# Kernel optimization log

Hardware: AMD Instinct MI355X
Metric: run time of the kernel (lower is better)

Reference implementation:

```python
import jax, jax.numpy as jnp
import numpy as np

# Config constants (match init_kwargs / config)
B = 16        # config.BATCH_SIZE
T = 2048      # config.TRAIN_LEN
C = 256       # input channels (input_shape[-1])
K = 8         # kernel_size
F = 256       # nb_filters
DIL = 4       # dilation_rate


def setup_inputs() -> dict:
    key = jax.random.key(0)
    k1, k2, k3 = jax.random.split(key, 3)
    inputs = jax.random.normal(k1, (B, T, C), dtype=jnp.float32)
    kernel = jax.random.normal(k2, (C, K, F), dtype=jnp.float32) * 0.05
    bias = jax.random.normal(k3, (F,), dtype=jnp.float32) * 0.05
    return {"inputs": inputs, "kernel": kernel, "bias": bias}


def reference(inputs, kernel, bias):
    # Original TF layer computes, per (b,t,k,f):
    #   raw[b,t,k,f] = sum_c (x[b,t,c] * kernel[c,k,f] + bias[f])
    #               = conv[b,t,k,f] + C * bias[f]
    # (bias is added BEFORE the reduce_sum over the channel axis, so it is
    #  scaled by C — we reproduce that quirk faithfully.)
    # Then each (t,k) slice is scatter-added to output time t + k*dilation
    # (the gather_nd + zero-pad construction in TF implements exactly this
    #  dilated transposed-conv scatter; non-matching positions gather zeros),
    # and finally the last T timesteps are kept.
    Bq, Tq, Cq = inputs.shape
    Kq, Fq = kernel.shape[1], kernel.shape[2]
    conv = jnp.einsum('btc,ckf->btkf', inputs, kernel) + jnp.asarray(Cq, inputs.dtype) * bias
    L = Tq + (Kq - 1) * DIL  # final_time_len
    # scatter positions: out[i + j*DIL] += conv[:, i, j, :]
    pos = (jnp.arange(Tq)[:, None] + DIL * jnp.arange(Kq)[None, :]).reshape(-1)  # (T*K,)
    out = jnp.zeros((Bq, L, Fq), dtype=conv.dtype)
    out = out.at[:, pos, :].add(conv.reshape(Bq, Tq * Kq, Fq))
    return out[:, -Tq:, :]
```

## Files before the change

### kernel.cpp

```cpp
#include <hip/hip_runtime.h>
#include <hip/hip_bf16.h>


#define B_   16
#define T_   2048
#define C_   256
#define KT   8
#define F_   256
#define SH   28
#define BT   128
#define WIN  (BT + SH)
#define AF32_OFF 0
#define ABF_OFF  19968
#define BB_OFF   39936

typedef __attribute__((ext_vector_type(8))) short short8;
typedef __attribute__((ext_vector_type(4))) float floatx4;

__device__ inline void gload16(const void* g, void* l) {
    __builtin_amdgcn_global_load_lds(
        (const __attribute__((address_space(1))) void*)g,
        (__attribute__((address_space(3))) void*)l, 16, 0, 0);
}

__device__ inline short8 cvt8(float4 a, float4 b) {
    float v[8] = {a.x, a.y, a.z, a.w, b.x, b.y, b.z, b.w};
    short8 r;
    #pragma unroll
    for (int i = 0; i < 8; ++i) {
        __hip_bfloat16 h = __float2bfloat16(v[i]);
        r[i] = *reinterpret_cast<const short*>(&h);
    }
    return r;
}

__global__ __launch_bounds__(256) void wprep_kernel(const float* __restrict__ W,
                                                    ushort* __restrict__ Wf) {
    const int o  = blockIdx.x * 256 + threadIdx.x;
    const int gg = o & 511;
    const int tf = o >> 9;
    const int fh = tf & 1;
    const int S  = tf >> 1;
    const int j  = S & 7, c = S >> 3;
    const int fl = gg >> 2, p = gg & 3;
    const int q  = p ^ ((fl >> 1) & 3);
    const int f  = fh * 128 + fl;
    const int c0 = c * 32 + q * 8;
    short8 pk;
    #pragma unroll
    for (int i = 0; i < 8; ++i) {
        __hip_bfloat16 h = __float2bfloat16(W[((c0 + i) * KT + j) * F_ + f]);
        pk[i] = *reinterpret_cast<const short*>(&h);
    }
    *reinterpret_cast<short8*>(Wf + (size_t)o * 8) = pk;
}

__global__ __launch_bounds__(256, 2) void deconv_kernel(
        const float* __restrict__ x, const ushort* __restrict__ Wf,
        const float* __restrict__ bias, float* __restrict__ out) {
    __shared__ alignas(16) char smem[64512];
    const int bid = blockIdx.x;
    const int fh  = bid & 1;
    const int tb  = bid >> 1;
    const int b   = tb & 15;
    const int t0  = (tb >> 4) * BT;
    const int tid = threadIdx.x;
    const int w   = tid >> 6, lane = tid & 63;
    const int l16 = lane & 15, q = lane >> 4;
    const int wm  = w >> 1, wf2 = w & 1;
    const int rA  = wm * 64 + l16;
    const int flb = wf2 * 64 + l16;

    float*  Af = (float*)(smem + AF32_OFF);
    ushort* Ab = (ushort*)(smem + ABF_OFF);
    ushort* Bb = (ushort*)(smem + BB_OFF);

#define VMW(N_) do { asm volatile("s_waitcnt vmcnt(" #N_ ")" ::: "memory"); \
        __builtin_amdgcn_sched_barrier(0); } while (0)
#define LKW() do { asm volatile("s_waitcnt lgkmcnt(0)" ::: "memory");       \
        __builtin_amdgcn_sched_barrier(0); } while (0)
#define BAR() do { __builtin_amdgcn_sched_barrier(0);                       \
        __builtin_amdgcn_s_barrier();                                       \
        asm volatile("" ::: "memory");                                      \
        __builtin_amdgcn_sched_barrier(0); } while (0)

#define A_ROUND(k_, cc_) do {                                               \
        const int u_ = (k_) * 256 + tid;                                    \
        if ((k_) < 4 || u_ < WIN * 8) {                                     \
            const int row_ = u_ >> 3, g_ = u_ & 7;                          \
            int tr_ = t0 + row_; if (tr_ > T_ - 1) tr_ = T_ - 1;            \
            const float* src_ = x + ((size_t)(b * T_ + tr_) * C_ +          \
                                     (cc_) * 32 + g_ * 4);                  \
            gload16(src_, smem + AF32_OFF + ((k_) * 256 + w * 64) * 16);    \
        } } while (0)

#define B_STAGE(S_) do {                                                    \
        const ushort* s0_ = Wf + (((size_t)(S_) * 2 + fh) * 4096);          \
        char* l0_ = smem + BB_OFF + ((S_) % 3) * 8192;                      \
        gload16(s0_ + tid * 8,         l0_ + (w * 64) * 16);                \
        gload16(s0_ + 2048 + tid * 8,  l0_ + (256 + w * 64) * 16);          \
        } while (0)

#define CVT_ROUND(r_, p2_) do {                                             \
        const int task_ = (r_) * 256 + tid;                                 \
        if ((r_) < 2 || task_ < WIN * 4) {                                  \
            const int row_ = task_ >> 2, qq_ = task_ & 3;                   \
            const int pp_ = (qq_ + row_) & 3;                               \
            short8 pk_ = {0, 0, 0, 0, 0, 0, 0, 0};                          \
            if (t0 + row_ < T_) {                                           \
                const float* fp_ = Af + row_ * 32 + pp_ * 8;                \
                float4 u0_ = *(const float4*)fp_;                           \
                float4 u1_ = *(const float4*)(fp_ + 4);                     \
                pk_ = cvt8(u0_, u1_);                                       \
            }                                                               \
            *(short8*)(Ab + (p2_) * 4992 + row_ * 32 +                      \
                       ((pp_ ^ ((row_ >> 1) & 3)) * 8)) = pk_;              \
        } } while (0)

#define MFMA_PHASE(c_, jj_) do {                                            \
        const ushort* ab_ = Ab + ((c_) & 1) * 4992;                         \
        const ushort* bb_ = Bb + ((((c_) * 8 + (jj_)) % 3)) * 4096;         \
        short8 afr_[4], bfr_[4];                                            \
        _Pragma("unroll")                                                   \
        for (int mf = 0; mf < 4; ++mf) {                                    \
            const int row_ = rA + (SH - 4 * (jj_)) + mf * 16;               \
            afr_[mf] = *(const short8*)(ab_ + row_ * 32 +                   \
                        ((q ^ ((row_ >> 1) & 3)) * 8));                     \
        }                                                                   \
        _Pragma("unroll")                                                   \
        for (int nf = 0; nf < 4; ++nf) {                                    \
            const int fl_ = flb + nf * 16;                                  \
            bfr_[nf] = *(const short8*)(bb_ + fl_ * 32 +                    \
                        ((q ^ ((fl_ >> 1) & 3)) * 8));                      \
        }                                                                   \
        __builtin_amdgcn_s_setprio(1);                                      \
        _Pragma("unroll")                                                   \
        for (int mf = 0; mf < 4; ++mf)                                      \
            _Pragma("unroll")                                               \
            for (int nf = 0; nf < 4; ++nf)                                  \
                acc[mf][nf] = __builtin_amdgcn_mfma_f32_16x16x32_bf16(      \
                    afr_[mf], bfr_[nf], acc[mf][nf], 0, 0, 0);              \
        __builtin_amdgcn_s_setprio(0);                                      \
        } while (0)

#define PHASE(jj_, NN_, DOA_, CV_) do {                                     \
        if (DOA_) A_ROUND(jj_, c + 1);                                      \
        B_STAGE(c * 8 + (jj_) + 2);                                         \
        VMW(NN_);                                                           \
        BAR();                                                              \
        MFMA_PHASE(c, jj_);                                                 \
        if ((CV_) == 1) { CVT_ROUND(0, (c + 1) & 1);                        \
                          CVT_ROUND(1, (c + 1) & 1); LKW(); }               \
        if ((CV_) == 2) { CVT_ROUND(2, (c + 1) & 1); LKW(); }               \
        BAR();                                                              \
        } while (0)

#define PHASE7(jj_, NN_, DOB_) do {                                         \
        if (DOB_) B_STAGE(56 + (jj_) + 2);                                  \
        VMW(NN_);                                                           \
        BAR();                                                              \
        MFMA_PHASE(7, jj_);                                                 \
        BAR();                                                              \
        } while (0)

    float bf4[4];
    #pragma unroll
    for (int nf = 0; nf < 4; ++nf) bf4[nf] = bias[fh * 128 + flb + nf * 16];

    floatx4 acc[4][4];
    #pragma unroll
    for (int mf = 0; mf < 4; ++mf)
        #pragma unroll
        for (int nf = 0; nf < 4; ++nf)
            acc[mf][nf] = (floatx4){0.f, 0.f, 0.f, 0.f};

    A_ROUND(0, 0); A_ROUND(1, 0); A_ROUND(2, 0); A_ROUND(3, 0); A_ROUND(4, 0);
    B_STAGE(0); B_STAGE(1);
    VMW(4);
    BAR();
    CVT_ROUND(0, 0); CVT_ROUND(1, 0); CVT_ROUND(2, 0);
    LKW();
    BAR();

    for (int c = 0; c < 7; ++c) {
        PHASE(0, 5, 1, 0);
        PHASE(1, 6, 1, 0);
        PHASE(2, 6, 1, 0);
        PHASE(3, 6, 1, 0);
        PHASE(4, 6, 1, 0);
        PHASE(5, 5, 0, 0);
        PHASE(6, 4, 0, 1);
        PHASE(7, 4, 0, 2);
    }
    PHASE7(0, 4, 1); PHASE7(1, 4, 1); PHASE7(2, 4, 1); PHASE7(3, 4, 1);
    PHASE7(4, 4, 1); PHASE7(5, 4, 1); PHASE7(6, 2, 0); PHASE7(7, 0, 0);

    #pragma unroll
    for (int mf = 0; mf < 4; ++mf) {
        #pragma unroll
        for (int nf = 0; nf < 4; ++nf) {
            const int f = fh * 128 + flb + nf * 16;
            #pragma unroll
            for (int r = 0; r < 4; ++r) {
                const int t = t0 + wm * 64 + mf * 16 + q * 4 + r;
                const int jmin = (t < T_ - SH) ? 0 : (((t - (T_ - SH)) >> 2) + 1);
                out[(size_t)(b * T_ + t) * F_ + f] =
                    acc[mf][nf][r] + (float)(8 - jmin) * 256.0f * bf4[nf];
            }
        }
    }
#undef VMW
#undef LKW
#undef BAR
#undef A_ROUND
#undef B_STAGE
#undef CVT_ROUND
#undef MFMA_PHASE
#undef PHASE
#undef PHASE7
}

extern "C" void kernel_launch(void* const* d_in, const int* in_sizes, int n_in,
                              void* d_out, int out_size, void* d_ws, size_t ws_size,
                              hipStream_t stream) {
    const float* x    = (const float*)d_in[0];
    const float* W    = (const float*)d_in[1];
    const float* bias = (const float*)d_in[2];
    float* out = (float*)d_out;
    ushort* Wf = (ushort*)d_ws;

    wprep_kernel<<<256, 256, 0, stream>>>(W, Wf);
    deconv_kernel<<<512, 256, 0, stream>>>(x, Wf, bias, out);
}
```

Before: 50.58 us.

## Stream weight fragments directly into registers and cut per-tap barriers

Weight fragments are now laid out by wprep in MFMA fragment order and loaded straight into registers with inline global_load_dwordx4, using a 3-slot register ring, instead of being staged through LDS. The fp32 input staging is double-buffered with a rotated layout, so only two barriers per channel chunk remain instead of two per tap. The bf16 conversion is spread across the last taps. This removes LDS traffic and most barrier stalls for B, at the cost of more VGPRs (48 extra for bR) and reliance on hand-counted vmcnt waits.

```diff
diff --git a/kernel.cpp b/kernel.cpp
--- a/kernel.cpp
+++ b/kernel.cpp
@@ -10,12 +10,13 @@
 #define SH   28
 #define BT   128
 #define WIN  (BT + SH)
-#define AF32_OFF 0
-#define ABF_OFF  19968
-#define BB_OFF   39936
+#define FB   19968
+#define ABFB 9984
+#define ABF  (2 * FB)
 
 typedef __attribute__((ext_vector_type(8))) short short8;
 typedef __attribute__((ext_vector_type(4))) float floatx4;
+typedef __attribute__((ext_vector_type(4))) int   intx4;
 
 __device__ inline void gload16(const void* g, void* l) {
     __builtin_amdgcn_global_load_lds(
@@ -36,29 +37,27 @@
 
 __global__ __launch_bounds__(256) void wprep_kernel(const float* __restrict__ W,
                                                     ushort* __restrict__ Wf) {
-    const int o  = blockIdx.x * 256 + threadIdx.x;
-    const int gg = o & 511;
-    const int tf = o >> 9;
-    const int fh = tf & 1;
-    const int S  = tf >> 1;
-    const int j  = S & 7, c = S >> 3;
-    const int fl = gg >> 2, p = gg & 3;
-    const int q  = p ^ ((fl >> 1) & 3);
-    const int f  = fh * 128 + fl;
-    const int c0 = c * 32 + q * 8;
+    const int tid  = threadIdx.x;
+    const int fid  = blockIdx.x * 4 + (tid >> 6);
+    const int lane = tid & 63;
+    const int g    = fid & 15;
+    const int S    = fid >> 4;
+    const int j    = S & 7, c = S >> 3;
+    const int c0   = c * 32 + (lane >> 4) * 8;
+    const int f    = g * 16 + (lane & 15);
     short8 pk;
     #pragma unroll
     for (int i = 0; i < 8; ++i) {
         __hip_bfloat16 h = __float2bfloat16(W[((c0 + i) * KT + j) * F_ + f]);
         pk[i] = *reinterpret_cast<const short*>(&h);
     }
-    *reinterpret_cast<short8*>(Wf + (size_t)o * 8) = pk;
+    *reinterpret_cast<short8*>(Wf + (size_t)fid * 512 + lane * 8) = pk;
 }
 
 __global__ __launch_bounds__(256, 2) void deconv_kernel(
         const float* __restrict__ x, const ushort* __restrict__ Wf,
         const float* __restrict__ bias, float* __restrict__ out) {
-    __shared__ alignas(16) char smem[64512];
+    __shared__ alignas(16) char smem[59904];
     const int bid = blockIdx.x;
     const int fh  = bid & 1;
     const int tb  = bid >> 1;
@@ -68,12 +67,8 @@
     const int w   = tid >> 6, lane = tid & 63;
     const int l16 = lane & 15, q = lane >> 4;
     const int wm  = w >> 1, wf2 = w & 1;
-    const int rA  = wm * 64 + l16;
-    const int flb = wf2 * 64 + l16;
-
-    float*  Af = (float*)(smem + AF32_OFF);
-    ushort* Ab = (ushort*)(smem + ABF_OFF);
-    ushort* Bb = (ushort*)(smem + BB_OFF);
+    const char* wfbase = (const char*)Wf +
+        (size_t)(fh * 8 + wf2 * 4) * 1024 + (size_t)lane * 16;
 
 #define VMW(N_) do { asm volatile("s_waitcnt vmcnt(" #N_ ")" ::: "memory"); \
         __builtin_amdgcn_sched_barrier(0); } while (0)
@@ -86,52 +81,50 @@
 
 #define A_ROUND(k_, cc_) do {                                               \
         const int u_ = (k_) * 256 + tid;                                    \
-        if ((k_) < 4 || u_ < WIN * 8) {                                     \
-            const int row_ = u_ >> 3, g_ = u_ & 7;                          \
+        if ((k_) < 4 || tid < 224) {                                        \
+            const int row_ = u_ >> 3, s_ = u_ & 7;                          \
+            const int v_   = (s_ + 8 - (row_ & 7)) & 7;                     \
             int tr_ = t0 + row_; if (tr_ > T_ - 1) tr_ = T_ - 1;            \
-            const float* src_ = x + ((size_t)(b * T_ + tr_) * C_ +          \
-                                     (cc_) * 32 + g_ * 4);                  \
-            gload16(src_, smem + AF32_OFF + ((k_) * 256 + w * 64) * 16);    \
+            gload16(x + ((size_t)(b * T_ + tr_) * C_ + (cc_) * 32 + v_ * 4),\
+                    smem + ((cc_) & 1) * FB + ((k_) * 256 + w * 64) * 16);  \
         } } while (0)
 
-#define B_STAGE(S_) do {                                                    \
-        const ushort* s0_ = Wf + (((size_t)(S_) * 2 + fh) * 4096);          \
-        char* l0_ = smem + BB_OFF + ((S_) % 3) * 8192;                      \
-        gload16(s0_ + tid * 8,         l0_ + (w * 64) * 16);                \
-        gload16(s0_ + 2048 + tid * 8,  l0_ + (256 + w * 64) * 16);          \
+#define B_ISSUE(S_, sl_) do {                                               \
+        const char* p_ = wfbase + (size_t)(S_) * 16384;                     \
+        asm volatile("global_load_dwordx4 %0, %1, off"                      \
+            : "=v"(bR[sl_][0]) : "v"(p_) : "memory");                       \
+        asm volatile("global_load_dwordx4 %0, %1, off offset:1024"          \
+            : "=v"(bR[sl_][1]) : "v"(p_) : "memory");                       \
+        asm volatile("global_load_dwordx4 %0, %1, off offset:2048"          \
+            : "=v"(bR[sl_][2]) : "v"(p_) : "memory");                       \
+        asm volatile("global_load_dwordx4 %0, %1, off offset:3072"          \
+            : "=v"(bR[sl_][3]) : "v"(p_) : "memory");                       \
         } while (0)
 
-#define CVT_ROUND(r_, p2_) do {                                             \
-        const int task_ = (r_) * 256 + tid;                                 \
-        if ((r_) < 2 || task_ < WIN * 4) {                                  \
-            const int row_ = task_ >> 2, qq_ = task_ & 3;                   \
-            const int pp_ = (qq_ + row_) & 3;                               \
-            short8 pk_ = {0, 0, 0, 0, 0, 0, 0, 0};                          \
-            if (t0 + row_ < T_) {                                           \
-                const float* fp_ = Af + row_ * 32 + pp_ * 8;                \
-                float4 u0_ = *(const float4*)fp_;                           \
-                float4 u1_ = *(const float4*)(fp_ + 4);                     \
-                pk_ = cvt8(u0_, u1_);                                       \
-            }                                                               \
-            *(short8*)(Ab + (p2_) * 4992 + row_ * 32 +                      \
-                       ((pp_ ^ ((row_ >> 1) & 3)) * 8)) = pk_;              \
+#define CVT_ROUND(r_, par_) do {                                            \
+        if ((r_) < 2 || tid < 112) {                                        \
+            const int task_ = (r_) * 256 + tid;                             \
+            const int row_ = task_ >> 2, g_ = task_ & 3;                    \
+            const int s1_ = (2 * g_ + row_) & 7;                            \
+            const int s2_ = (2 * g_ + 1 + row_) & 7;                        \
+            const char* fb_ = smem + (par_) * FB;                           \
+            float4 u0_ = *(const float4*)(fb_ + (row_ * 8 + s1_) * 16);     \
+            float4 u1_ = *(const float4*)(fb_ + (row_ * 8 + s2_) * 16);     \
+            short8 pk_ = {0,0,0,0,0,0,0,0};                                 \
+            if (t0 + row_ < T_) pk_ = cvt8(u0_, u1_);                       \
+            const int p_ = g_ ^ ((row_ >> 1) & 3);                          \
+            *(short8*)(smem + ABF + (par_) * ABFB + (row_ * 4 + p_) * 16)   \
+                = pk_;                                                      \
         } } while (0)
 
-#define MFMA_PHASE(c_, jj_) do {                                            \
-        const ushort* ab_ = Ab + ((c_) & 1) * 4992;                         \
-        const ushort* bb_ = Bb + ((((c_) * 8 + (jj_)) % 3)) * 4096;         \
-        short8 afr_[4], bfr_[4];                                            \
+#define MFMA_TAP(c_, j_) do {                                               \
+        const char* ab_ = smem + ABF + ((c_) & 1) * ABFB;                   \
+        short8 af_[4];                                                      \
         _Pragma("unroll")                                                   \
         for (int mf = 0; mf < 4; ++mf) {                                    \
-            const int row_ = rA + (SH - 4 * (jj_)) + mf * 16;               \
-            afr_[mf] = *(const short8*)(ab_ + row_ * 32 +                   \
-                        ((q ^ ((row_ >> 1) & 3)) * 8));                     \
-        }                                                                   \
-        _Pragma("unroll")                                                   \
-        for (int nf = 0; nf < 4; ++nf) {                                    \
-            const int fl_ = flb + nf * 16;                                  \
-            bfr_[nf] = *(const short8*)(bb_ + fl_ * 32 +                    \
-                        ((q ^ ((fl_ >> 1) & 3)) * 8));                      \
+            const int row_ = wm * 64 + (SH - 4 * (j_)) + mf * 16 + l16;     \
+            const int p_   = q ^ ((row_ >> 1) & 3);                         \
+            af_[mf] = *(const short8*)(ab_ + (row_ * 4 + p_) * 16);         \
         }                                                                   \
         __builtin_amdgcn_s_setprio(1);                                      \
         _Pragma("unroll")                                                   \
@@ -139,33 +132,34 @@
             _Pragma("unroll")                                               \
             for (int nf = 0; nf < 4; ++nf)                                  \
                 acc[mf][nf] = __builtin_amdgcn_mfma_f32_16x16x32_bf16(      \
-                    afr_[mf], bfr_[nf], acc[mf][nf], 0, 0, 0);              \
+                    af_[mf],                                                \
+                    *(short8*)&bR[(((c_) * 8 + (j_)) % 3)][nf],             \
+                    acc[mf][nf], 0, 0, 0);                                  \
         __builtin_amdgcn_s_setprio(0);                                      \
         } while (0)
 
-#define PHASE(jj_, NN_, DOA_, CV_) do {                                     \
-        if (DOA_) A_ROUND(jj_, c + 1);                                      \
-        B_STAGE(c * 8 + (jj_) + 2);                                         \
-        VMW(NN_);                                                           \
+#define CHUNK_STD(c_) do {                                                  \
+        A_ROUND(0, (c_)+1); A_ROUND(1, (c_)+1); A_ROUND(2, (c_)+1);         \
+        A_ROUND(3, (c_)+1); A_ROUND(4, (c_)+1);                             \
+        B_ISSUE((c_)*8+2, (((c_)*8+2)%3)); VMW(13); MFMA_TAP(c_, 0);        \
+        B_ISSUE((c_)*8+3, (((c_)*8+3)%3)); VMW(13); MFMA_TAP(c_, 1);        \
+        B_ISSUE((c_)*8+4, (((c_)*8+4)%3)); VMW(8);  MFMA_TAP(c_, 2);        \
         BAR();                                                              \
-        MFMA_PHASE(c, jj_);                                                 \
-        if ((CV_) == 1) { CVT_ROUND(0, (c + 1) & 1);                        \
-                          CVT_ROUND(1, (c + 1) & 1); LKW(); }               \
-        if ((CV_) == 2) { CVT_ROUND(2, (c + 1) & 1); LKW(); }               \
-        BAR();                                                              \
+        B_ISSUE((c_)*8+5, (((c_)*8+5)%3)); VMW(8);  MFMA_TAP(c_, 3);        \
+        B_ISSUE((c_)*8+6, (((c_)*8+6)%3)); VMW(8);  MFMA_TAP(c_, 4);        \
+        B_ISSUE((c_)*8+7, (((c_)*8+7)%3)); VMW(8);  MFMA_TAP(c_, 5);        \
+        CVT_ROUND(0, ((c_)+1)&1);                                           \
+        B_ISSUE((c_)*8+8, (((c_)*8+8)%3)); VMW(8);  MFMA_TAP(c_, 6);        \
+        CVT_ROUND(1, ((c_)+1)&1);                                           \
+        B_ISSUE((c_)*8+9, (((c_)*8+9)%3)); VMW(8);  MFMA_TAP(c_, 7);        \
+        CVT_ROUND(2, ((c_)+1)&1);                                           \
+        LKW(); BAR();                                                       \
         } while (0)
 
-#define PHASE7(jj_, NN_, DOB_) do {                                         \
-        if (DOB_) B_STAGE(56 + (jj_) + 2);                                  \
-        VMW(NN_);                                                           \
-        BAR();                                                              \
-        MFMA_PHASE(7, jj_);                                                 \
-        BAR();                                                              \
-        } while (0)
-
     float bf4[4];
     #pragma unroll
-    for (int nf = 0; nf < 4; ++nf) bf4[nf] = bias[fh * 128 + flb + nf * 16];
+    for (int nf = 0; nf < 4; ++nf)
+        bf4[nf] = bias[fh * 128 + wf2 * 64 + nf * 16 + l16];
 
     floatx4 acc[4][4];
     #pragma unroll
@@ -174,32 +168,32 @@
         for (int nf = 0; nf < 4; ++nf)
             acc[mf][nf] = (floatx4){0.f, 0.f, 0.f, 0.f};
 
+    intx4 bR[3][4];
+
     A_ROUND(0, 0); A_ROUND(1, 0); A_ROUND(2, 0); A_ROUND(3, 0); A_ROUND(4, 0);
-    B_STAGE(0); B_STAGE(1);
-    VMW(4);
+    B_ISSUE(0, 0); B_ISSUE(1, 1);
+    VMW(8);
     BAR();
     CVT_ROUND(0, 0); CVT_ROUND(1, 0); CVT_ROUND(2, 0);
-    LKW();
-    BAR();
-
-    for (int c = 0; c < 7; ++c) {
-        PHASE(0, 5, 1, 0);
-        PHASE(1, 6, 1, 0);
-        PHASE(2, 6, 1, 0);
-        PHASE(3, 6, 1, 0);
-        PHASE(4, 6, 1, 0);
-        PHASE(5, 5, 0, 0);
-        PHASE(6, 4, 0, 1);
-        PHASE(7, 4, 0, 2);
-    }
-    PHASE7(0, 4, 1); PHASE7(1, 4, 1); PHASE7(2, 4, 1); PHASE7(3, 4, 1);
-    PHASE7(4, 4, 1); PHASE7(5, 4, 1); PHASE7(6, 2, 0); PHASE7(7, 0, 0);
+    LKW(); BAR();
+
+    CHUNK_STD(0); CHUNK_STD(1); CHUNK_STD(2); CHUNK_STD(3);
+    CHUNK_STD(4); CHUNK_STD(5); CHUNK_STD(6);
+
+    B_ISSUE(58, (58 % 3)); VMW(8); MFMA_TAP(7, 0);
+    B_ISSUE(59, (59 % 3)); VMW(8); MFMA_TAP(7, 1);
+    B_ISSUE(60, (60 % 3)); VMW(8); MFMA_TAP(7, 2);
+    B_ISSUE(61, (61 % 3)); VMW(8); MFMA_TAP(7, 3);
+    B_ISSUE(62, (62 % 3)); VMW(8); MFMA_TAP(7, 4);
+    B_ISSUE(63, (63 % 3)); VMW(8); MFMA_TAP(7, 5);
+    VMW(4); MFMA_TAP(7, 6);
+    VMW(0); MFMA_TAP(7, 7);
 
     #pragma unroll
     for (int mf = 0; mf < 4; ++mf) {
         #pragma unroll
         for (int nf = 0; nf < 4; ++nf) {
-            const int f = fh * 128 + flb + nf * 16;
+            const int f = fh * 128 + wf2 * 64 + nf * 16 + l16;
             #pragma unroll
             for (int r = 0; r < 4; ++r) {
                 const int t = t0 + wm * 64 + mf * 16 + q * 4 + r;
@@ -213,11 +207,10 @@
 #undef LKW
 #undef BAR
 #undef A_ROUND
-#undef B_STAGE
+#undef B_ISSUE
 #undef CVT_ROUND
-#undef MFMA_PHASE
-#undef PHASE
-#undef PHASE7
+#undef MFMA_TAP
+#undef CHUNK_STD
 }
 
 extern "C" void kernel_launch(void* const* d_in, const int* in_sizes, int n_in,
```

After: 44.24 us. -12.5%, faster.
